# Kernel tuning notes

Hardware: AMD Instinct MI355X
Metric: run time of the kernel (lower is better)

## Reference

```python
import jax, jax.numpy as jnp
import numpy as np

NEG_INF = -1.0e12  # matches torch's -1e12 mask value
LEAKY_SLOPE = 0.01  # nn.LeakyReLU default


def setup_inputs() -> dict:
    key = jax.random.key(0)
    k1, k2, k3, k4 = jax.random.split(key, 4)
    B, N, in_c, out_c = 8, 2048, 64, 64
    inp = jax.random.normal(k1, (B, N, in_c), dtype=jnp.float32)
    adj = jax.random.randint(k2, (B, N, N), 0, 2, dtype=jnp.int32)
    W = jax.random.normal(k3, (in_c, out_c), dtype=jnp.float32) * (1.0 / np.sqrt(in_c))
    a = jax.random.normal(k4, (2 * out_c, 1), dtype=jnp.float32) * 0.1
    return {"inp": inp, "adj": adj, "W": W, "a": a}


def reference(inp, adj, W, a):
    # GAT layer. The original builds an O(B*N^2*2*out_c) concat tensor;
    # a^T [h_i || h_j] decomposes exactly into (h_i . a1) + (h_j . a2).
    out_c = W.shape[1]
    h = jnp.einsum('bni,io->bno', inp, W)          # [B,N,out_c]
    a1 = a[:out_c, 0]                               # [out_c]
    a2 = a[out_c:, 0]                               # [out_c]
    e_i = h @ a1                                    # [B,N] source term
    e_j = h @ a2                                    # [B,N] target term
    e = e_i[:, :, None] + e_j[:, None, :]           # [B,N,N]
    e = jnp.where(e > 0, e, LEAKY_SLOPE * e)        # LeakyReLU(0.01)
    masked = jnp.where(adj > 0, e, NEG_INF)
    attention = jax.nn.softmax(masked, axis=2)      # [B,N,N]
    # dropout omitted (eval mode / deterministic reference)
    h_prime = jnp.einsum('bnm,bmo->bno', attention, h)  # [B,N,out_c]
    return h_prime
```

## Files before the change

### kernel.cpp

```cpp
#include <hip/hip_runtime.h>
#include <cstdint>

#define BB 8
#define NN 2048
#define CC 64
#define TI 64
#define JSPLIT 2
#define KRANGE (NN / JSPLIT)
#define JCH 128
#define NCH (KRANGE / JCH)

typedef __attribute__((ext_vector_type(8))) __bf16 bf16x8;
typedef __attribute__((ext_vector_type(4))) float f32x4;
typedef __attribute__((ext_vector_type(4))) unsigned int u32x4;
typedef __attribute__((ext_vector_type(4))) int i32x4;

static const size_t WS_H   = 0;
static const size_t WS_E1  = WS_H  + (size_t)BB*NN*CC;
static const size_t WS_E2  = WS_E1 + (size_t)BB*NN;
static const size_t WS_HT  = WS_E2 + (size_t)BB*NN;
static const size_t WS_ACC = WS_HT + (size_t)BB*CC*NN;
static const size_t WS_Z   = WS_ACC + (size_t)JSPLIT*BB*NN*CC;

#define GL16(g, l) __builtin_amdgcn_global_load_lds( \
    (const __attribute__((address_space(1))) void*)(g), \
    (__attribute__((address_space(3))) void*)(uint32_t)(uintptr_t)(l), 16, 0, 0)
#define GL4(g, l) __builtin_amdgcn_global_load_lds( \
    (const __attribute__((address_space(1))) void*)(g), \
    (__attribute__((address_space(3))) void*)(uint32_t)(uintptr_t)(l), 4, 0, 0)
#define WAIT18() asm volatile("s_waitcnt vmcnt(18)" ::: "memory")
#define WAIT0()  asm volatile("s_waitcnt vmcnt(0)" ::: "memory")
#define BAR()    __builtin_amdgcn_s_barrier()

__global__ __launch_bounds__(256) void k1_proj(const float* __restrict__ inp,
        const float* __restrict__ Wm, const float* __restrict__ av,
        float* __restrict__ h, float* __restrict__ e1, float* __restrict__ e2) {
    __shared__ float inp_lds[256];
    int t = threadIdx.x;
    size_t base = (size_t)blockIdx.x * 256;
    inp_lds[t] = inp[base + t];
    __syncthreads();
    int r = t >> 6;
    int c = t & 63;
    const float* irow = &inp_lds[r * 64];
    float acc = 0.f;
    #pragma unroll
    for (int k = 0; k < 64; k++) acc = fmaf(irow[k], Wm[k * 64 + c], acc);
    size_t row = (size_t)blockIdx.x * 4 + r;
    h[row * 64 + c] = acc;
    float v1 = acc * av[c];
    float v2 = acc * av[64 + c];
    #pragma unroll
    for (int o = 32; o > 0; o >>= 1) {
        v1 += __shfl_down(v1, o);
        v2 += __shfl_down(v2, o);
    }
    if (c == 0) { e1[row] = v1; e2[row] = v2; }
}

__global__ __launch_bounds__(256) void k1b_transpose(const float* __restrict__ h,
        unsigned short* __restrict__ hiT, unsigned short* __restrict__ loT) {
    __shared__ float tile[64][65];
    int t = threadIdx.x;
    int b = blockIdx.x >> 5;
    int i0 = (blockIdx.x & 31) * 64;
    const float* hb = h + ((size_t)b * NN + i0) * CC;
    #pragma unroll
    for (int q = 0; q < 16; q++) {
        int idx = q * 256 + t;
        tile[idx >> 6][idx & 63] = hb[idx];
    }
    __syncthreads();
    int c = t & 63;
    int rgrp = t >> 6;
    unsigned int uh[8], ul[8];
    #pragma unroll
    for (int p = 0; p < 8; p++) {
        unsigned int pack_h = 0, pack_l = 0;
        #pragma unroll
        for (int s = 0; s < 2; s++) {
            float v = tile[rgrp * 16 + p * 2 + s][c];
            __bf16 bh = (__bf16)v;
            float fh = (float)bh;
            __bf16 bl = (__bf16)(v - fh);
            unsigned int ubh = (unsigned int)__builtin_bit_cast(unsigned short, bh);
            unsigned int ubl = (unsigned int)__builtin_bit_cast(unsigned short, bl);
            pack_h |= ubh << (16 * s);
            pack_l |= ubl << (16 * s);
        }
        uh[p] = pack_h; ul[p] = pack_l;
    }
    size_t off = ((size_t)b * 64 + c) * NN + i0 + rgrp * 16;
    u32x4* dh = (u32x4*)(hiT + off);
    u32x4* dl = (u32x4*)(loT + off);
    dh[0] = u32x4{uh[0], uh[1], uh[2], uh[3]};
    dh[1] = u32x4{uh[4], uh[5], uh[6], uh[7]};
    dl[0] = u32x4{ul[0], ul[1], ul[2], ul[3]};
    dl[1] = u32x4{ul[4], ul[5], ul[6], ul[7]};
}

__global__ __launch_bounds__(256) void k2_mfma(const int* __restrict__ adj,
        const unsigned short* __restrict__ hiT, const unsigned short* __restrict__ loT,
        const float* __restrict__ e1, const float* __restrict__ e2,
        float* __restrict__ accp, float* __restrict__ zp) {
    __shared__ __align__(16) char smem[2 * 32768 + 2 * 512];
    char* hi0 = smem;
    char* lo0 = smem + 16384;
    char* hi1 = smem + 32768;
    char* lo1 = smem + 49152;
    char* e2L0 = smem + 65536;
    char* e2L1 = smem + 66048;

    int bid = blockIdx.x;
    int b    = bid & 7;
    int rest = bid >> 3;
    int s    = rest & (JSPLIT - 1);
    int tile = rest >> 1;
    int i0 = tile * TI;
    int jbase = s * KRANGE;

    int t = threadIdx.x;
    int w = t >> 6;
    int l = t & 63;
    int col = l & 15;
    int kg  = l >> 4;

    int wlo = (w >> 1);
    int cw  = (w & 1) * 32;
    int l4  = l >> 4;
    int sl  = l & 15;
    int wq_off = (w & 1) * 8192;

    const int* adjrow = adj + ((size_t)b * NN + i0 + w * 16 + col) * NN;
    float e1v = e1[(size_t)b * NN + i0 + w * 16 + col];
    const float* e2b = e2 + (size_t)b * NN;
    const unsigned short* hiTb = hiT + (size_t)b * 64 * NN;
    const unsigned short* loTb = loT + (size_t)b * 64 * NN;
    const unsigned short* sTb = wlo ? loTb : hiTb;

    f32x4 acc[4];
    #pragma unroll
    for (int n = 0; n < 4; n++) acc[n] = f32x4{0.f, 0.f, 0.f, 0.f};
    f32x4 accZ = f32x4{0.f, 0.f, 0.f, 0.f};

    __bf16 onev = (__bf16)1.0f, zerov = (__bf16)0.0f;
    bf16x8 onesf;
    #pragma unroll
    for (int i = 0; i < 8; i++) onesf[i] = (col == 0) ? onev : zerov;

    i32x4 aA[8], aB[8];

#define STAGE(jcN, B) { \
    int j0s = jbase + (jcN) * JCH; \
    char* lb = (wlo ? ((B) ? lo1 : lo0) : ((B) ? hi1 : hi0)) + wq_off; \
    _Pragma("unroll") \
    for (int q = 0; q < 8; q++) { \
        int c = cw + q * 4 + l4; \
        const unsigned short* src = sTb + (size_t)c * NN + j0s + ((sl ^ (c & 7)) << 3); \
        GL16(src, lb + q * 1024); \
    } \
    GL4(e2b + j0s + l, ((B) ? e2L1 : e2L0)); \
    GL4(e2b + j0s + 64 + l, ((B) ? e2L1 : e2L0) + 256); \
}

#define ADJP(jcN, arr) { \
    int j0a = jbase + (jcN) * JCH; \
    _Pragma("unroll") \
    for (int ks = 0; ks < 4; ks++) { \
        const i32x4* ap = (const i32x4*)(adjrow + j0a + ks * 32 + kg * 8); \
        arr[2 * ks]     = ap[0]; \
        arr[2 * ks + 1] = ap[1]; \
    } \
}

#define COMPUTE(B, arr) { \
    const char* hiLb = (B) ? hi1 : hi0; \
    const char* loLb = (B) ? lo1 : lo0; \
    const float* e2c = (const float*)((B) ? e2L1 : e2L0); \
    _Pragma("unroll") \
    for (int ks = 0; ks < 4; ks++) { \
        int krel = ks * 32 + kg * 8; \
        i32x4 a0 = arr[2 * ks]; \
        i32x4 a1 = arr[2 * ks + 1]; \
        f32x4 e20 = *(const f32x4*)(e2c + krel); \
        f32x4 e21 = *(const f32x4*)(e2c + krel + 4); \
        float xs[8] = {e20.x, e20.y, e20.z, e20.w, e21.x, e21.y, e21.z, e21.w}; \
        int ms[8] = {a0.x, a0.y, a0.z, a0.w, a1.x, a1.y, a1.z, a1.w}; \
        bf16x8 pf; \
        _Pragma("unroll") \
        for (int i = 0; i < 8; i++) { \
            float x = e1v + xs[i]; \
            x = fmaxf(x, 0.01f * x); \
            x = __expf(x); \
            x = (ms[i] > 0) ? x : 0.0f; \
            pf[i] = (__bf16)x; \
        } \
        int seg = ks * 4 + kg; \
        _Pragma("unroll") \
        for (int n = 0; n < 4; n++) { \
            int c = n * 16 + col; \
            int boff = c * 256 + ((seg ^ (c & 7)) << 4); \
            bf16x8 bhi = __builtin_bit_cast(bf16x8, *(const f32x4*)(hiLb + boff)); \
            bf16x8 blo = __builtin_bit_cast(bf16x8, *(const f32x4*)(loLb + boff)); \
            acc[n] = __builtin_amdgcn_mfma_f32_16x16x32_bf16(pf, bhi, acc[n], 0, 0, 0); \
            acc[n] = __builtin_amdgcn_mfma_f32_16x16x32_bf16(pf, blo, acc[n], 0, 0, 0); \
        } \
        accZ = __builtin_amdgcn_mfma_f32_16x16x32_bf16(pf, onesf, accZ, 0, 0, 0); \
    } \
}

    STAGE(0, 0);
    ADJP(0, aA);

    #pragma unroll
    for (int jc = 0; jc < NCH; jc += 2) {
        STAGE(jc + 1, 1);
        ADJP(jc + 1, aB);
        WAIT18();
        BAR();
        COMPUTE(0, aA);
        BAR();
        if (jc + 2 < NCH) {
            STAGE(jc + 2, 0);
            ADJP(jc + 2, aA);
            WAIT18();
        } else {
            WAIT0();
        }
        BAR();
        COMPUTE(1, aB);
        BAR();
    }

    size_t orow = (size_t)s * BB * NN + (size_t)b * NN + i0 + w * 16 + kg * 4;
    float* accout = accp + orow * CC;
    #pragma unroll
    for (int n = 0; n < 4; n++) {
        #pragma unroll
        for (int r = 0; r < 4; r++) {
            accout[(size_t)r * CC + n * 16 + col] = acc[n][r];
        }
    }
    if (col == 0) {
        #pragma unroll
        for (int r = 0; r < 4; r++) zp[orow + r] = accZ[r];
    }
#undef STAGE
#undef ADJP
#undef COMPUTE
}

__global__ __launch_bounds__(256) void k3_final(const float* __restrict__ accp,
        const float* __restrict__ zp, float* __restrict__ out) {
    int idx = blockIdx.x * 256 + threadIdx.x;
    const int TOT4 = BB * NN * CC / 4;
    if (idx >= TOT4) return;
    int row = idx >> 4;
    f32x4 s0 = ((const f32x4*)accp)[idx];
    f32x4 s1 = ((const f32x4*)accp)[idx + TOT4];
    float z = zp[row] + zp[row + BB * NN];
    float inv = (z > 0.f) ? (1.0f / z) : 0.f;
    f32x4 o;
    o.x = (s0.x + s1.x) * inv;
    o.y = (s0.y + s1.y) * inv;
    o.z = (s0.z + s1.z) * inv;
    o.w = (s0.w + s1.w) * inv;
    ((f32x4*)out)[idx] = o;
}

extern "C" void kernel_launch(void* const* d_in, const int* in_sizes, int n_in,
                              void* d_out, int out_size, void* d_ws, size_t ws_size,
                              hipStream_t stream) {
    const float* inp = (const float*)d_in[0];
    const int*   adj = (const int*)d_in[1];
    const float* Wm  = (const float*)d_in[2];
    const float* av  = (const float*)d_in[3];
    float* ws = (float*)d_ws;
    float* h    = ws + WS_H;
    float* e1   = ws + WS_E1;
    float* e2   = ws + WS_E2;
    unsigned short* hiT = (unsigned short*)(ws + WS_HT);
    unsigned short* loT = hiT + (size_t)BB * CC * NN;
    float* accp = ws + WS_ACC;
    float* zp   = ws + WS_Z;
    float* out  = (float*)d_out;

    k1_proj<<<BB * NN / 4, 256, 0, stream>>>(inp, Wm, av, h, e1, e2);
    k1b_transpose<<<BB * (NN / 64), 256, 0, stream>>>(h, hiT, loT);
    k2_mfma<<<BB * 32 * JSPLIT, 256, 0, stream>>>(adj, hiT, loT, e1, e2, accp, zp);
    k3_final<<<(BB * NN * CC / 4 + 255) / 256, 256, 0, stream>>>(accp, zp, out);
}
```

Measured before the change: 53.50 us.

## Fuse split-K reduction into MFMA kernel via in-block LDS reduction

Each block now runs 512 threads and handles both halves of the neighbour range itself. The two wave groups combine their partial accumulators and softmax denominators through LDS, then write the normalised output directly. This drops the final reduction kernel and the global round trip of partial sums. In exchange the block count halves, each block uses about 130KB of LDS so only one block fits per CU, and the end of the kernel gains extra barriers.

Measured after the change: 53.22 us. Within noise of the previous version (-0.5%).

```diff
diff --git a/kernel.cpp b/kernel.cpp
--- a/kernel.cpp
+++ b/kernel.cpp
@@ -5,10 +5,8 @@
 #define NN 2048
 #define CC 64
 #define TI 64
-#define JSPLIT 2
-#define KRANGE (NN / JSPLIT)
 #define JCH 128
-#define NCH (KRANGE / JCH)
+#define NCH 8
 
 typedef __attribute__((ext_vector_type(8))) __bf16 bf16x8;
 typedef __attribute__((ext_vector_type(4))) float f32x4;
@@ -19,8 +17,6 @@
 static const size_t WS_E1  = WS_H  + (size_t)BB*NN*CC;
 static const size_t WS_E2  = WS_E1 + (size_t)BB*NN;
 static const size_t WS_HT  = WS_E2 + (size_t)BB*NN;
-static const size_t WS_ACC = WS_HT + (size_t)BB*CC*NN;
-static const size_t WS_Z   = WS_ACC + (size_t)JSPLIT*BB*NN*CC;
 
 #define GL16(g, l) __builtin_amdgcn_global_load_lds( \
     (const __attribute__((address_space(1))) void*)(g), \
@@ -99,40 +95,35 @@
     dl[1] = u32x4{ul[4], ul[5], ul[6], ul[7]};
 }
 
-__global__ __launch_bounds__(256) void k2_mfma(const int* __restrict__ adj,
+__global__ __launch_bounds__(512, 1) void k2_mfma(const int* __restrict__ adj,
         const unsigned short* __restrict__ hiT, const unsigned short* __restrict__ loT,
         const float* __restrict__ e1, const float* __restrict__ e2,
-        float* __restrict__ accp, float* __restrict__ zp) {
-    __shared__ __align__(16) char smem[2 * 32768 + 2 * 512];
-    char* hi0 = smem;
-    char* lo0 = smem + 16384;
-    char* hi1 = smem + 32768;
-    char* lo1 = smem + 49152;
-    char* e2L0 = smem + 65536;
-    char* e2L1 = smem + 66048;
+        float* __restrict__ out) {
+    __shared__ __align__(16) char smem[133120];
 
     int bid = blockIdx.x;
     int b    = bid & 7;
-    int rest = bid >> 3;
-    int s    = rest & (JSPLIT - 1);
-    int tile = rest >> 1;
+    int tile = bid >> 3;
     int i0 = tile * TI;
-    int jbase = s * KRANGE;
 
     int t = threadIdx.x;
     int w = t >> 6;
+    int hw = w >> 2;
+    int wl = w & 3;
     int l = t & 63;
     int col = l & 15;
     int kg  = l >> 4;
-
-    int wlo = (w >> 1);
-    int cw  = (w & 1) * 32;
+    int jbase = hw * 1024;
+
+    int wlo = wl >> 1;
+    int cw  = (wl & 1) * 32;
     int l4  = l >> 4;
     int sl  = l & 15;
-    int wq_off = (w & 1) * 8192;
-
-    const int* adjrow = adj + ((size_t)b * NN + i0 + w * 16 + col) * NN;
-    float e1v = e1[(size_t)b * NN + i0 + w * 16 + col];
+    int wq_off = (wl & 1) * 8192;
+    int half_off = hw * 65536;
+
+    const int* adjrow = adj + ((size_t)b * NN + i0 + wl * 16 + col) * NN;
+    float e1v = e1[(size_t)b * NN + i0 + wl * 16 + col];
     const float* e2b = e2 + (size_t)b * NN;
     const unsigned short* hiTb = hiT + (size_t)b * 64 * NN;
     const unsigned short* loTb = loT + (size_t)b * 64 * NN;
@@ -152,15 +143,16 @@
 
 #define STAGE(jcN, B) { \
     int j0s = jbase + (jcN) * JCH; \
-    char* lb = (wlo ? ((B) ? lo1 : lo0) : ((B) ? hi1 : hi0)) + wq_off; \
+    char* lb = smem + half_off + (wlo ? 16384 : 0) + ((B) ? 32768 : 0) + wq_off; \
     _Pragma("unroll") \
     for (int q = 0; q < 8; q++) { \
         int c = cw + q * 4 + l4; \
         const unsigned short* src = sTb + (size_t)c * NN + j0s + ((sl ^ (c & 7)) << 3); \
         GL16(src, lb + q * 1024); \
     } \
-    GL4(e2b + j0s + l, ((B) ? e2L1 : e2L0)); \
-    GL4(e2b + j0s + 64 + l, ((B) ? e2L1 : e2L0) + 256); \
+    char* e2d = smem + 131072 + hw * 1024 + ((B) ? 512 : 0); \
+    GL4(e2b + j0s + l, e2d); \
+    GL4(e2b + j0s + 64 + l, e2d + 256); \
 }
 
 #define ADJP(jcN, arr) { \
@@ -174,9 +166,9 @@
 }
 
 #define COMPUTE(B, arr) { \
-    const char* hiLb = (B) ? hi1 : hi0; \
-    const char* loLb = (B) ? lo1 : lo0; \
-    const float* e2c = (const float*)((B) ? e2L1 : e2L0); \
+    const char* hiLb = smem + half_off + ((B) ? 32768 : 0); \
+    const char* loLb = hiLb + 16384; \
+    const float* e2c = (const float*)(smem + 131072 + hw * 1024 + ((B) ? 512 : 0)); \
     _Pragma("unroll") \
     for (int ks = 0; ks < 4; ks++) { \
         int krel = ks * 32 + kg * 8; \
@@ -232,40 +224,43 @@
         BAR();
     }
 
-    size_t orow = (size_t)s * BB * NN + (size_t)b * NN + i0 + w * 16 + kg * 4;
-    float* accout = accp + orow * CC;
-    #pragma unroll
-    for (int n = 0; n < 4; n++) {
+    float* red  = (float*)(smem + 65536 + wl * 4096);
+    float* zred = (float*)(smem + 81920);
+    if (hw == 1) {
+        #pragma unroll
+        for (int n = 0; n < 4; n++)
+            #pragma unroll
+            for (int r = 0; r < 4; r++)
+                red[(kg * 4 + r) * 64 + n * 16 + col] = acc[n][r];
+        if (col == 0) {
+            #pragma unroll
+            for (int r = 0; r < 4; r++) zred[wl * 16 + kg * 4 + r] = accZ[r];
+        }
+    }
+    BAR();
+    if (hw == 0 && col == 0) {
         #pragma unroll
         for (int r = 0; r < 4; r++) {
-            accout[(size_t)r * CC + n * 16 + col] = acc[n][r];
-        }
-    }
-    if (col == 0) {
-        #pragma unroll
-        for (int r = 0; r < 4; r++) zp[orow + r] = accZ[r];
+            float zt = accZ[r] + zred[wl * 16 + kg * 4 + r];
+            zred[wl * 16 + kg * 4 + r] = (zt > 0.f) ? 1.0f / zt : 0.f;
+        }
+    }
+    BAR();
+    if (hw == 0) {
+        float* outb = out + ((size_t)b * NN + i0 + wl * 16) * CC;
+        #pragma unroll
+        for (int r = 0; r < 4; r++) {
+            float zi = zred[wl * 16 + kg * 4 + r];
+            #pragma unroll
+            for (int n = 0; n < 4; n++) {
+                float v = (acc[n][r] + red[(kg * 4 + r) * 64 + n * 16 + col]) * zi;
+                outb[(size_t)(kg * 4 + r) * CC + n * 16 + col] = v;
+            }
+        }
     }
 #undef STAGE
 #undef ADJP
 #undef COMPUTE
-}
-
-__global__ __launch_bounds__(256) void k3_final(const float* __restrict__ accp,
-        const float* __restrict__ zp, float* __restrict__ out) {
-    int idx = blockIdx.x * 256 + threadIdx.x;
-    const int TOT4 = BB * NN * CC / 4;
-    if (idx >= TOT4) return;
-    int row = idx >> 4;
-    f32x4 s0 = ((const f32x4*)accp)[idx];
-    f32x4 s1 = ((const f32x4*)accp)[idx + TOT4];
-    float z = zp[row] + zp[row + BB * NN];
-    float inv = (z > 0.f) ? (1.0f / z) : 0.f;
-    f32x4 o;
-    o.x = (s0.x + s1.x) * inv;
-    o.y = (s0.y + s1.y) * inv;
-    o.z = (s0.z + s1.z) * inv;
-    o.w = (s0.w + s1.w) * inv;
-    ((f32x4*)out)[idx] = o;
 }
 
 extern "C" void kernel_launch(void* const* d_in, const int* in_sizes, int n_in,
@@ -281,12 +276,9 @@
     float* e2   = ws + WS_E2;
     unsigned short* hiT = (unsigned short*)(ws + WS_HT);
     unsigned short* loT = hiT + (size_t)BB * CC * NN;
-    float* accp = ws + WS_ACC;
-    float* zp   = ws + WS_Z;
     float* out  = (float*)d_out;
 
     k1_proj<<<BB * NN / 4, 256, 0, stream>>>(inp, Wm, av, h, e1, e2);
     k1b_transpose<<<BB * (NN / 64), 256, 0, stream>>>(h, hiT, loT);
-    k2_mfma<<<BB * 32 * JSPLIT, 256, 0, stream>>>(adj, hiT, loT, e1, e2, accp, zp);
-    k3_final<<<(BB * NN * CC / 4 + 255) / 256, 256, 0, stream>>>(accp, zp, out);
-}
+    k2_mfma<<<BB * (NN / TI), 512, 0, stream>>>(adj, hiT, loT, e1, e2, out);
+}
```
